# Kernel optimization log

Hardware: AMD Instinct MI355X
Metric: run time of the kernel (lower is better)

Reference implementation:

```python
import jax, jax.numpy as jnp
import numpy as np

NTYPES = 2
B, N, MNEI = 4, 512, 100
M = MNEI * NTYPES          # neighbor slots = maxNeighborNum * ntypes
EMB_LAST = 100             # embedding net sizes [25, 50, 100]
FIT_H = 240
M2 = 16
RMIN, RMAX = 0.5, 6.0


def setup_inputs():
    key = jax.random.key(0)
    ks = jax.random.split(key, 24)
    r = jax.random.uniform(ks[0], (B, N, M), minval=0.6, maxval=7.0)
    v = jax.random.normal(ks[1], (B, N, M, 3))
    v = v / jnp.linalg.norm(v, axis=-1, keepdims=True)
    keep = jax.random.uniform(ks[2], (B, N, M)) < 0.7
    ImageDR = jnp.concatenate([r[..., None], r[..., None] * v], axis=-1)
    ImageDR = jnp.where(keep[..., None], ImageDR, 0.0).astype(jnp.float32)
    Imagetype_map = jax.random.randint(ks[3], (N,), 0, NTYPES)
    list_neigh = jax.random.randint(ks[4], (B, N, M), 0, N + 1)
    type_map = jnp.arange(NTYPES)
    davg = (0.01 * jax.random.normal(ks[5], (NTYPES, M, 4))).astype(jnp.float32)
    dstd = (1.0 + 0.1 * jax.random.uniform(ks[6], (NTYPES, M, 4))).astype(jnp.float32)

    def w(k, shape, fan):
        return (jax.random.normal(k, shape) / np.sqrt(fan)).astype(jnp.float32)

    def b(k, shape):
        return (0.1 * jax.random.normal(k, shape)).astype(jnp.float32)

    emb_W0 = w(ks[7], (NTYPES, NTYPES, 1, 25), 1)
    emb_b0 = b(ks[8], (NTYPES, NTYPES, 25))
    emb_W1 = w(ks[9], (NTYPES, NTYPES, 25, 50), 25)
    emb_b1 = b(ks[10], (NTYPES, NTYPES, 50))
    emb_W2 = w(ks[11], (NTYPES, NTYPES, 50, 100), 50)
    emb_b2 = b(ks[12], (NTYPES, NTYPES, 100))
    fin = M2 * EMB_LAST
    fit_W0 = w(ks[13], (NTYPES, fin, FIT_H), fin)
    fit_b0 = b(ks[14], (NTYPES, FIT_H))
    fit_W1 = w(ks[15], (NTYPES, FIT_H, FIT_H), FIT_H)
    fit_b1 = b(ks[16], (NTYPES, FIT_H))
    fit_W2 = w(ks[17], (NTYPES, FIT_H, FIT_H), FIT_H)
    fit_b2 = b(ks[18], (NTYPES, FIT_H))
    fit_W3 = w(ks[19], (NTYPES, FIT_H, 1), FIT_H)
    fit_b3 = b(ks[20], (NTYPES, 1))
    energy_shift = jnp.array([-3.37, -5.21], dtype=jnp.float32)
    return dict(list_neigh=list_neigh, Imagetype_map=Imagetype_map, type_map=type_map,
                ImageDR=ImageDR, nghost=0, davg=davg, dstd=dstd,
                emb_W0=emb_W0, emb_b0=emb_b0, emb_W1=emb_W1, emb_b1=emb_b1,
                emb_W2=emb_W2, emb_b2=emb_b2,
                fit_W0=fit_W0, fit_b0=fit_b0, fit_W1=fit_W1, fit_b1=fit_b1,
                fit_W2=fit_W2, fit_b2=fit_b2, fit_W3=fit_W3, fit_b3=fit_b3,
                energy_shift=energy_shift)


def _emb(s, W0, b0, W1, b1, W2, b2):
    # DeepPot-SE embedding net with doubling resnet connections
    h = jnp.tanh(s @ W0 + b0)                                   # [..., 25]
    h = jnp.tanh(h @ W1 + b1) + jnp.concatenate([h, h], -1)     # [..., 50]
    return jnp.tanh(h @ W2 + b2) + jnp.concatenate([h, h], -1)  # [..., 100]


def _fit(d, W0, b0, W1, b1, W2, b2, W3, b3):
    h = jnp.tanh(d @ W0 + b0)
    h = h + jnp.tanh(h @ W1 + b1)
    h = h + jnp.tanh(h @ W2 + b2)
    return h @ W3 + b3


def _forward(ImageDR, davg, dstd,
             emb_W0, emb_b0, emb_W1, emb_b1, emb_W2, emb_b2,
             fit_W0, fit_b0, fit_W1, fit_b1, fit_W2, fit_b2, fit_W3, fit_b3,
             energy_shift, Imagetype_map):
    Bsz, Nat, Mtot, _ = ImageDR.shape
    m = Mtot // NTYPES
    R = ImageDR[..., 0]
    Rsafe = jnp.where(R > 1e-5, R, 1.0)
    # smooth switching function s(r): 1/r below Rmin, polynomial taper to Rmax
    u = (R - RMIN) / (RMAX - RMIN)
    mid = (u ** 3 * (-6.0 * u * u + 15.0 * u - 10.0) + 1.0) / Rsafe
    S = jnp.where((R > 0) & (R < RMIN), 1.0 / Rsafe,
                  jnp.where((R > RMIN) & (R < RMAX), mid, 0.0))
    msk = (jnp.abs(R) > 1e-5)[..., None]
    Ri = jnp.concatenate([S[..., None],
                          jnp.where(msk, (S / Rsafe)[..., None] * ImageDR[..., 1:4], 0.0)],
                         axis=-1)                                    # [B,N,M,4] = (s, s*x/r, s*y/r, s*z/r)
    # per-center-type normalization (irregular gather of stats)
    Rn = (Ri - davg[Imagetype_map][None]) / dstd[Imagetype_map][None]
    tmask = [(Imagetype_map == i).astype(Rn.dtype)[None, :, None, None] for i in range(NTYPES)]
    xyz = jnp.zeros((Bsz, Nat, 4, EMB_LAST), Rn.dtype)
    for j in range(NTYPES):                                          # neighbor-type slice
        sl = Rn[:, :, j * m:(j + 1) * m, :]                          # [B,N,m,4]
        s = sl[..., 0:1]
        G = jnp.zeros(sl.shape[:3] + (EMB_LAST,), sl.dtype)
        for i in range(NTYPES):                                      # center type -> pair net (i, j)
            G = G + tmask[i] * _emb(s, emb_W0[i, j], emb_b0[i, j],
                                    emb_W1[i, j], emb_b1[i, j], emb_W2[i, j], emb_b2[i, j])
        xyz = xyz + jnp.einsum('bnmk,bnmc->bnkc', sl, G)
    xyz = xyz / (m * NTYPES)
    # descriptor D = (Ri^T G)^T (Ri^T G)[:, :M2], flattened -> [B,N,EMB_LAST*M2]
    D = jnp.einsum('bnkc,bnkd->bncd', xyz, xyz[..., :M2]).reshape(Bsz, Nat, -1)
    Ei = jnp.zeros((Bsz, Nat), D.dtype)
    for i in range(NTYPES):
        e = _fit(D, fit_W0[i], fit_b0[i], fit_W1[i], fit_b1[i],
                 fit_W2[i], fit_b2[i], fit_W3[i], fit_b3[i])[..., 0] + energy_shift[i]
        Ei = Ei + tmask[i][:, :, 0, 0] * e
    Etot = jnp.sum(Ei, axis=1)
    return Etot, Ei


def reference(list_neigh, Imagetype_map, type_map, ImageDR, nghost, davg, dstd,
              emb_W0, emb_b0, emb_W1, emb_b1, emb_W2, emb_b2,
              fit_W0, fit_b0, fit_W1, fit_b1, fit_W2, fit_b2, fit_W3, fit_b3,
              energy_shift):
    return _forward(ImageDR, davg, dstd,
                    emb_W0, emb_b0, emb_W1, emb_b1, emb_W2, emb_b2,
                    fit_W0, fit_b0, fit_W1, fit_b1, fit_W2, fit_b2, fit_W3, fit_b3,
                    energy_shift, Imagetype_map)
```

## Files before the change

### kernel.cpp

```cpp
#include <hip/hip_runtime.h>
#include <math.h>

#define NT 2
#define BSZ 4
#define NAT 512
#define NATOMS 2048
#define NNEI 200
#define EMB 100
#define FITH 240
#define DDIM 1600
#define TBK 1024

#define BIAS_F  16
#define W3C_F   (BIAS_F + 3 * 512)
#define USH_BYTE 8320
#define TBL_U   0
#define W0T_U   409600
#define W1T_U   (W0T_U + 819200)
#define W2T_U   (W1T_U + 262144)
#define D_U     (W2T_U + 262144)
#define H0_U    (D_U + 3276800)
#define H1_U    (H0_U + 1048576)
#define USH_END (H1_U + 1048576)
#define WS_NEED ((size_t)USH_BYTE + (size_t)USH_END * 2)

typedef short s8v __attribute__((ext_vector_type(8)));
typedef float f4v __attribute__((ext_vector_type(4)));

__device__ __forceinline__ float ftanh(float x) {
    float ax = fabsf(x);
    float e = __expf(2.0f * ax);
    float t = 1.0f - __fdividef(2.0f, e + 1.0f);
    return (x < 0.0f) ? -t : t;
}
__device__ __forceinline__ unsigned short f2bf(float f) {
    unsigned u = __float_as_uint(f);
    u += 0x7FFFu + ((u >> 16) & 1u);
    return (unsigned short)(u >> 16);
}
__device__ __forceinline__ float bf2f(unsigned short s) {
    return __uint_as_float(((unsigned)s) << 16);
}
__device__ __forceinline__ float calc_S(float R) {
    float Rsafe = (R > 1e-5f) ? R : 1.0f;
    float u = (R - 0.5f) * (1.0f / 5.5f);
    float uu = u * u;
    float mid = (u * uu * (-6.0f * uu + 15.0f * u - 10.0f) + 1.0f) / Rsafe;
    float S = 0.0f;
    if (R > 0.0f && R < 0.5f)      S = 1.0f / Rsafe;
    else if (R > 0.5f && R < 6.0f) S = mid;
    return S;
}

#define N_W0 819200
#define N_W1 262144
#define N_W2 262144
#define N_B  1536
#define N_W3 512
#define N_EI 2048
__global__ void wtrans_kernel(const float* __restrict__ fW0, const float* __restrict__ fW1,
                              const float* __restrict__ fW2,
                              const float* __restrict__ fb0, const float* __restrict__ fb1,
                              const float* __restrict__ fb2,
                              const float* __restrict__ fW3, const float* __restrict__ fb3,
                              const float* __restrict__ eshift, const int* __restrict__ itype,
                              float* __restrict__ ws, float* __restrict__ out) {
    unsigned short* u0 = (unsigned short*)((char*)ws + USH_BYTE);
    int id = blockIdx.x * 256 + threadIdx.x;
    if (id < N_W0) {
        int n = id / 1600, k = id - n * 1600;
        float v = 0.0f;
        if (n < 240)                  v = fW0[(size_t)k * 240 + n];
        else if (n >= 256 && n < 496) v = fW0[(size_t)(1600 + k) * 240 + (n - 256)];
        u0[W0T_U + id] = f2bf(v);
        return;
    }
    id -= N_W0;
    if (id < N_W1) {
        int n = id / 512, k = id - n * 512;
        float v = 0.0f;
        if (n < 240 && k < 240)       v = fW1[(size_t)k * 240 + n];
        else if (n >= 256 && n < 496 && k >= 256 && k < 496)
                                      v = fW1[(size_t)(240 + (k - 256)) * 240 + (n - 256)];
        u0[W1T_U + id] = f2bf(v);
        return;
    }
    id -= N_W1;
    if (id < N_W2) {
        int n = id / 512, k = id - n * 512;
        float v = 0.0f;
        if (n < 240 && k < 240)       v = fW2[(size_t)k * 240 + n];
        else if (n >= 256 && n < 496 && k >= 256 && k < 496)
                                      v = fW2[(size_t)(240 + (k - 256)) * 240 + (n - 256)];
        u0[W2T_U + id] = f2bf(v);
        return;
    }
    id -= N_W2;
    if (id < N_B) {
        int l = id / 512, n = id - l * 512;
        const float* fb = (l == 0) ? fb0 : (l == 1) ? fb1 : fb2;
        float v = 0.0f;
        if (n < 240)                  v = fb[n];
        else if (n >= 256 && n < 496) v = fb[240 + (n - 256)];
        ws[BIAS_F + l * 512 + n] = v;
        return;
    }
    id -= N_B;
    if (id < N_W3) {
        int n = id;
        float v = 0.0f;
        if (n < 240)                  v = fW3[n];
        else if (n >= 256 && n < 496) v = fW3[240 + (n - 256)];
        ws[W3C_F + n] = v;
        return;
    }
    id -= N_W3;
    if (id < N_EI) {
        int t = itype[id & (NAT - 1)];
        out[4 + id] = fb3[t] + eshift[t];
    }
}

__global__ void __launch_bounds__(256) table_kernel(
    const float* __restrict__ davg, const float* __restrict__ dstd,
    const float* __restrict__ eW0, const float* __restrict__ eb0,
    const float* __restrict__ eW1, const float* __restrict__ eb1,
    const float* __restrict__ eW2, const float* __restrict__ eb2,
    float* __restrict__ ws)
{
    __shared__ float los[100], his[100];
    __shared__ float rng[2];
    __shared__ float h0s[8][25];
    __shared__ float h1s[8][50];
    const int bx = blockIdx.x;
    const int nid = bx >> 7;
    const int kb  = (bx & 127) * 8;
    const int t = nid >> 1, j = nid & 1;
    const int tid = threadIdx.x;

    if (tid < 100) {
        int m = j * 100 + tid;
        float av = davg[(t * NNEI + m) * 4];
        float sd = dstd[(t * NNEI + m) * 4];
        float inv = __fdividef(1.0f, sd);
        float a = (0.0f - av) * inv;
        float b = (2.0f - av) * inv;
        los[tid] = fminf(a, b);
        his[tid] = fmaxf(a, b);
    }
    __syncthreads();
    if (tid == 0) {
        float lo = los[0], hi = his[0];
        for (int i = 1; i < 100; ++i) { lo = fminf(lo, los[i]); hi = fmaxf(hi, his[i]); }
        rng[0] = lo; rng[1] = hi - lo;
        if (kb == 0) {
            ws[nid * 2] = lo;
            ws[nid * 2 + 1] = (float)(TBK - 1) / (hi - lo);
        }
    }
    __syncthreads();
    const float smin = rng[0], span = rng[1];
    const float* W0 = eW0 + nid * 25;
    const float* B0 = eb0 + nid * 25;
    if (tid < 200) {
        int q = tid / 25, a = tid % 25;
        float s = smin + span * ((float)(kb + q) * (1.0f / (TBK - 1)));
        h0s[q][a] = ftanh(fmaf(s, W0[a], B0[a]));
    }
    __syncthreads();
    const float* W1 = eW1 + nid * 1250;
    const float* B1 = eb1 + nid * 50;
    for (int idx = tid; idx < 400; idx += 256) {
        int q = idx / 50, cc = idx % 50;
        float acc = B1[cc];
#pragma unroll
        for (int a = 0; a < 25; ++a) acc = fmaf(h0s[q][a], W1[a * 50 + cc], acc);
        h1s[q][cc] = ftanh(acc) + h0s[q][(cc < 25) ? cc : cc - 25];
    }
    __syncthreads();
    const float* W2 = eW2 + nid * 5000;
    const float* B2 = eb2 + nid * 100;
    unsigned short* tblu = (unsigned short*)((char*)ws + USH_BYTE) + TBL_U;
    for (int idx = tid; idx < 800; idx += 256) {
        int q = idx / 100, c = idx % 100;
        float acc = B2[c];
#pragma unroll
        for (int a = 0; a < 50; ++a) acc = fmaf(h1s[q][a], W2[a * 100 + c], acc);
        float g = ftanh(acc) + h1s[q][(c < 50) ? c : c - 50];
        tblu[(size_t)(nid * TBK + kb + q) * 100 + c] = f2bf(g);
    }
}

__global__ void __launch_bounds__(128) embed_kernel(
    const int* __restrict__ itype, const float* __restrict__ imagedr,
    const float* __restrict__ davg, const float* __restrict__ dstd,
    float* __restrict__ ws)
{
    __shared__ __align__(16) float4 srn[NNEI];
    __shared__ float sx[NNEI];
    __shared__ float part[2][400];
    const int atom = blockIdx.x;
    const int n = atom & (NAT - 1);
    const int tid = threadIdx.x;
    const int t = itype[n];
    unsigned short* u0 = (unsigned short*)((char*)ws + USH_BYTE);

    const float sm0 = ws[(t * 2 + 0) * 2], sc0 = ws[(t * 2 + 0) * 2 + 1];
    const float sm1 = ws[(t * 2 + 1) * 2], sc1 = ws[(t * 2 + 1) * 2 + 1];

    for (int m = tid; m < NNEI; m += 128) {
        float4 dr = ((const float4*)imagedr)[(size_t)atom * NNEI + m];
        float R = dr.x;
        float S = calc_S(R);
        float Rsafe = (R > 1e-5f) ? R : 1.0f;
        float sr = (fabsf(R) > 1e-5f) ? (S / Rsafe) : 0.0f;
        float4 av = ((const float4*)davg)[t * NNEI + m];
        float4 sd = ((const float4*)dstd)[t * NNEI + m];
        float4 rv;
        rv.x = (S         - av.x) / sd.x;
        rv.y = (sr * dr.y - av.y) / sd.y;
        rv.z = (sr * dr.z - av.z) / sd.z;
        rv.w = (sr * dr.w - av.w) / sd.w;
        srn[m] = rv;
        float smin = (m >= 100) ? sm1 : sm0;
        float scal = (m >= 100) ? sc1 : sc0;
        sx[m] = fminf(fmaxf((rv.x - smin) * scal, 0.0f), (float)(TBK - 2) + 0.9999f);
    }
    __syncthreads();

    const int w = tid >> 6, lane = tid & 63;
    const unsigned short* T = u0 + TBL_U + (size_t)(t * 2 + w) * TBK * EMB;
    const bool hi = (lane < 36);
    float xA0 = 0, xA1 = 0, xA2 = 0, xA3 = 0;
    float xB0 = 0, xB1 = 0, xB2 = 0, xB3 = 0;
#pragma unroll 4
    for (int mi = 0; mi < 100; ++mi) {
        int m = w * 100 + mi;
        float4 rv = srn[m];
        float x = sx[m];
        int i = (int)x;
        float f = x - (float)i;
        const unsigned short* Tr = T + (size_t)i * EMB;
        float g0 = bf2f(Tr[lane]);
        float g1 = bf2f(Tr[EMB + lane]);
        float g = fmaf(f, g1 - g0, g0);
        xA0 = fmaf(rv.x, g, xA0); xA1 = fmaf(rv.y, g, xA1);
        xA2 = fmaf(rv.z, g, xA2); xA3 = fmaf(rv.w, g, xA3);
        if (hi) {
            float h0v = bf2f(Tr[64 + lane]);
            float h1v = bf2f(Tr[EMB + 64 + lane]);
            float g2 = fmaf(f, h1v - h0v, h0v);
            xB0 = fmaf(rv.x, g2, xB0); xB1 = fmaf(rv.y, g2, xB1);
            xB2 = fmaf(rv.z, g2, xB2); xB3 = fmaf(rv.w, g2, xB3);
        }
    }
    part[w][0 * 100 + lane] = xA0; part[w][1 * 100 + lane] = xA1;
    part[w][2 * 100 + lane] = xA2; part[w][3 * 100 + lane] = xA3;
    if (hi) {
        part[w][0 * 100 + 64 + lane] = xB0; part[w][1 * 100 + 64 + lane] = xB1;
        part[w][2 * 100 + 64 + lane] = xB2; part[w][3 * 100 + 64 + lane] = xB3;
    }
    __syncthreads();
    const float inv = 1.0f / 200.0f;
    for (int idx = tid; idx < 400; idx += 128)
        part[0][idx] = (part[0][idx] + part[1][idx]) * inv;
    __syncthreads();
    unsigned short* Drow = u0 + D_U + (size_t)atom * DDIM;
    const float* xt = part[0];
    for (int idx = tid; idx < DDIM; idx += 128) {
        int c = idx >> 4, d = idx & 15;
        float s = xt[c] * xt[d] + xt[100 + c] * xt[100 + d]
                + xt[200 + c] * xt[200 + d] + xt[300 + c] * xt[300 + d];
        Drow[idx] = f2bf(s);
    }
}

__global__ void __launch_bounds__(128) gemm0_kernel(
    const unsigned short* __restrict__ A,
    const unsigned short* __restrict__ BT,
    const float* __restrict__ bias,
    unsigned short* __restrict__ Out)
{
    __shared__ float lred[64][17];
    const int tid = threadIdx.x;
    const int w = tid >> 6, lane = tid & 63;
    const int mr = lane & 15, q = lane >> 4;
    const int n0 = blockIdx.x * 64;
    const int m0 = blockIdx.y * 16;
    const unsigned short* Ap = A  + (size_t)(m0 + mr) * DDIM + w * 800 + q * 8;
    const unsigned short* Bp = BT + (size_t)(n0 + mr) * DDIM + w * 800 + q * 8;

    f4v a0 = {0,0,0,0}, a1 = {0,0,0,0}, a2 = {0,0,0,0}, a3 = {0,0,0,0};
#pragma unroll 5
    for (int kt = 0; kt < 25; ++kt) {
        s8v av = *(const s8v*)(Ap + kt * 32);
        s8v b0 = *(const s8v*)(Bp + kt * 32);
        s8v b1 = *(const s8v*)(Bp + 16 * DDIM + kt * 32);
        s8v b2 = *(const s8v*)(Bp + 32 * DDIM + kt * 32);
        s8v b3 = *(const s8v*)(Bp + 48 * DDIM + kt * 32);
        a0 = __builtin_amdgcn_mfma_f32_16x16x32_bf16(av, b0, a0, 0, 0, 0);
        a1 = __builtin_amdgcn_mfma_f32_16x16x32_bf16(av, b1, a1, 0, 0, 0);
        a2 = __builtin_amdgcn_mfma_f32_16x16x32_bf16(av, b2, a2, 0, 0, 0);
        a3 = __builtin_amdgcn_mfma_f32_16x16x32_bf16(av, b3, a3, 0, 0, 0);
    }
    if (w == 1) {
#pragma unroll
        for (int r = 0; r < 4; ++r) {
            lred[lane][r]      = a0[r];
            lred[lane][4 + r]  = a1[r];
            lred[lane][8 + r]  = a2[r];
            lred[lane][12 + r] = a3[r];
        }
    }
    __syncthreads();
    if (w == 0) {
#pragma unroll
        for (int j = 0; j < 4; ++j) {
            const int col = n0 + j * 16 + mr;
            const float bv = bias[col];
            f4v* ap = (j == 0) ? &a0 : (j == 1) ? &a1 : (j == 2) ? &a2 : &a3;
#pragma unroll
            for (int r = 0; r < 4; ++r) {
                float s = (*ap)[r] + lred[lane][j * 4 + r] + bv;
                int row = m0 + q * 4 + r;
                Out[(size_t)row * 512 + col] = f2bf(ftanh(s));
            }
        }
    }
}

__global__ void __launch_bounds__(64) gemmr_kernel(
    const unsigned short* __restrict__ A, const unsigned short* __restrict__ BT,
    const float* __restrict__ bias, const unsigned short* __restrict__ Res,
    unsigned short* __restrict__ Out,
    const float* __restrict__ w3c, const int* __restrict__ itype,
    float* __restrict__ out, int mode)
{
    const int lane = threadIdx.x;
    const int mr = lane & 15, q = lane >> 4;
    const int bx = blockIdx.x;
    const int n0 = bx * 64;
    const int m0 = blockIdx.y * 16;
    const int k0 = (bx >= 4) ? 256 : 0;
    const unsigned short* Ap = A  + (size_t)(m0 + mr) * 512 + k0 + q * 8;
    const unsigned short* Bp = BT + (size_t)(n0 + mr) * 512 + k0 + q * 8;

    f4v a0 = {0,0,0,0}, a1 = {0,0,0,0}, a2 = {0,0,0,0}, a3 = {0,0,0,0};
#pragma unroll
    for (int kt = 0; kt < 8; ++kt) {
        s8v av = *(const s8v*)(Ap + kt * 32);
        s8v b0 = *(const s8v*)(Bp + kt * 32);
        s8v b1 = *(const s8v*)(Bp + 16 * 512 + kt * 32);
        s8v b2 = *(const s8v*)(Bp + 32 * 512 + kt * 32);
        s8v b3 = *(const s8v*)(Bp + 48 * 512 + kt * 32);
        a0 = __builtin_amdgcn_mfma_f32_16x16x32_bf16(av, b0, a0, 0, 0, 0);
        a1 = __builtin_amdgcn_mfma_f32_16x16x32_bf16(av, b1, a1, 0, 0, 0);
        a2 = __builtin_amdgcn_mfma_f32_16x16x32_bf16(av, b2, a2, 0, 0, 0);
        a3 = __builtin_amdgcn_mfma_f32_16x16x32_bf16(av, b3, a3, 0, 0, 0);
    }
    const float bv0 = bias[n0 + mr],      bv1 = bias[n0 + 16 + mr];
    const float bv2 = bias[n0 + 32 + mr], bv3 = bias[n0 + 48 + mr];
    if (mode == 1) {
#pragma unroll
        for (int r = 0; r < 4; ++r) {
            int row = m0 + q * 4 + r;
            size_t base = (size_t)row * 512 + n0 + mr;
            Out[base]      = f2bf(bf2f(Res[base])      + ftanh(a0[r] + bv0));
            Out[base + 16] = f2bf(bf2f(Res[base + 16]) + ftanh(a1[r] + bv1));
            Out[base + 32] = f2bf(bf2f(Res[base + 32]) + ftanh(a2[r] + bv2));
            Out[base + 48] = f2bf(bf2f(Res[base + 48]) + ftanh(a3[r] + bv3));
        }
    } else {
        const int seg = (bx >= 4);
        const float w30 = w3c[n0 + mr],      w31 = w3c[n0 + 16 + mr];
        const float w32 = w3c[n0 + 32 + mr], w33 = w3c[n0 + 48 + mr];
#pragma unroll
        for (int r = 0; r < 4; ++r) {
            int row = m0 + q * 4 + r;
            size_t base = (size_t)row * 512 + n0 + mr;
            float p = (bf2f(Res[base])      + ftanh(a0[r] + bv0)) * w30
                    + (bf2f(Res[base + 16]) + ftanh(a1[r] + bv1)) * w31
                    + (bf2f(Res[base + 32]) + ftanh(a2[r] + bv2)) * w32
                    + (bf2f(Res[base + 48]) + ftanh(a3[r] + bv3)) * w33;
            p += __shfl_xor(p, 1, 16);
            p += __shfl_xor(p, 2, 16);
            p += __shfl_xor(p, 4, 16);
            p += __shfl_xor(p, 8, 16);
            if (mr == 0 && itype[row & (NAT - 1)] == seg)
                atomicAdd(&out[4 + row], p);
        }
    }
}

__global__ void etot_kernel(float* __restrict__ out) {
    const int b = blockIdx.x;
    float s = 0.0f;
    for (int n = threadIdx.x; n < NAT; n += 256) s += out[4 + b * NAT + n];
#pragma unroll
    for (int off = 32; off > 0; off >>= 1) s += __shfl_down(s, off, 64);
    __shared__ float rr[4];
    if ((threadIdx.x & 63) == 0) rr[threadIdx.x >> 6] = s;
    __syncthreads();
    if (threadIdx.x == 0) out[b] = rr[0] + rr[1] + rr[2] + rr[3];
}

__global__ void dp_atom_kernel(
    const int* __restrict__ itype, const float* __restrict__ imagedr,
    const float* __restrict__ davg, const float* __restrict__ dstd,
    const float* __restrict__ eW0, const float* __restrict__ eb0,
    const float* __restrict__ eW1, const float* __restrict__ eb1,
    const float* __restrict__ eW2, const float* __restrict__ eb2,
    const float* __restrict__ fW0, const float* __restrict__ fb0,
    const float* __restrict__ fW1, const float* __restrict__ fb1,
    const float* __restrict__ fW2, const float* __restrict__ fb2,
    const float* __restrict__ fW3, const float* __restrict__ fb3,
    const float* __restrict__ eshift, float* __restrict__ out)
{
    __shared__ __align__(16) float4 rn4[NNEI];
    __shared__ __align__(16) float  xyz[4 * EMB];
    __shared__ __align__(16) float  h0s[100 * 25];
    __shared__ __align__(16) float  smem[100 * 52];
    const int atom = blockIdx.x;
    const int n = atom & (NAT - 1);
    const int tid = threadIdx.x;
    const int t = itype[n];
    for (int m = tid; m < NNEI; m += 256) {
        float4 dr = ((const float4*)imagedr)[(size_t)atom * NNEI + m];
        float R = dr.x;
        float S = calc_S(R);
        float Rsafe = (R > 1e-5f) ? R : 1.0f;
        float sr = (fabsf(R) > 1e-5f) ? (S / Rsafe) : 0.0f;
        float4 av = ((const float4*)davg)[t * NNEI + m];
        float4 sd = ((const float4*)dstd)[t * NNEI + m];
        float4 rv;
        rv.x = (S - av.x) / sd.x; rv.y = (sr * dr.y - av.y) / sd.y;
        rv.z = (sr * dr.z - av.z) / sd.z; rv.w = (sr * dr.w - av.w) / sd.w;
        rn4[m] = rv;
    }
    const int c = tid & 127; const int mh = tid >> 7;
    float xp0 = 0, xp1 = 0, xp2 = 0, xp3 = 0;
    for (int j = 0; j < NT; ++j) {
        const int wb = t * NT + j;
        const float* W0 = eW0 + wb * 25; const float* B0 = eb0 + wb * 25;
        const float* W1 = eW1 + wb * 1250; const float* B1 = eb1 + wb * 50;
        const float* W2 = eW2 + wb * 5000; const float* B2 = eb2 + wb * 100;
        __syncthreads();
        for (int idx = tid; idx < 2500; idx += 256) {
            int m = idx / 25, a = idx - m * 25;
            h0s[idx] = ftanh(fmaf(rn4[j * 100 + m].x, W0[a], B0[a]));
        }
        __syncthreads();
        for (int idx = tid; idx < 5000; idx += 256) {
            int m = idx / 50, cc = idx - m * 50;
            const float* h0m = h0s + m * 25;
            float acc = B1[cc];
#pragma unroll
            for (int a = 0; a < 25; ++a) acc = fmaf(h0m[a], W1[a * 50 + cc], acc);
            smem[m * 52 + cc] = ftanh(acc) + h0m[(cc < 25) ? cc : cc - 25];
        }
        for (int idx = tid; idx < 200; idx += 256)
            smem[(idx >> 1) * 52 + 50 + (idx & 1)] = 0.0f;
        __syncthreads();
        if (c < EMB) {
            float w2c[52];
#pragma unroll
            for (int a = 0; a < 50; ++a) w2c[a] = W2[a * EMB + c];
            w2c[50] = 0; w2c[51] = 0;
            const float bc = B2[c];
            const int sk = (c < 50) ? c : c - 50;
            for (int i = 0; i < 50; ++i) {
                int m = mh * 50 + i;
                const float* h1m = smem + m * 52;
                float acc = bc;
#pragma unroll
                for (int q = 0; q < 13; ++q) {
                    float4 hv = ((const float4*)h1m)[q];
                    acc = fmaf(hv.x, w2c[4 * q], acc); acc = fmaf(hv.y, w2c[4 * q + 1], acc);
                    acc = fmaf(hv.z, w2c[4 * q + 2], acc); acc = fmaf(hv.w, w2c[4 * q + 3], acc);
                }
                float g = ftanh(acc) + h1m[sk];
                float4 rm = rn4[j * 100 + m];
                xp0 = fmaf(rm.x, g, xp0); xp1 = fmaf(rm.y, g, xp1);
                xp2 = fmaf(rm.z, g, xp2); xp3 = fmaf(rm.w, g, xp3);
            }
        }
    }
    __syncthreads();
    const float inv = 1.0f / 200.0f;
    if (mh == 0 && c < EMB) {
        xyz[c] = xp0 * inv; xyz[EMB + c] = xp1 * inv;
        xyz[2 * EMB + c] = xp2 * inv; xyz[3 * EMB + c] = xp3 * inv;
    }
    __syncthreads();
    if (mh == 1 && c < EMB) {
        xyz[c] += xp0 * inv; xyz[EMB + c] += xp1 * inv;
        xyz[2 * EMB + c] += xp2 * inv; xyz[3 * EMB + c] += xp3 * inv;
    }
    __syncthreads();
    float* Dld = smem;
    for (int idx = tid; idx < DDIM; idx += 256) {
        int cc = idx >> 4, d = idx & 15;
        Dld[idx] = xyz[cc] * xyz[d] + xyz[EMB + cc] * xyz[EMB + d]
                 + xyz[2 * EMB + cc] * xyz[2 * EMB + d] + xyz[3 * EMB + cc] * xyz[3 * EMB + d];
    }
    __syncthreads();
    float* hA = smem + DDIM; float* hB = hA + FITH; float* h2 = hB + FITH; float* red = h2 + FITH;
    if (tid < FITH) {
        const float* W = fW0 + (size_t)t * DDIM * FITH;
        float acc = fb0[t * FITH + tid];
        for (int f = 0; f < DDIM; f += 4) {
            float4 dv = *(const float4*)(Dld + f);
            acc = fmaf(dv.x, W[f * FITH + tid], acc); acc = fmaf(dv.y, W[(f + 1) * FITH + tid], acc);
            acc = fmaf(dv.z, W[(f + 2) * FITH + tid], acc); acc = fmaf(dv.w, W[(f + 3) * FITH + tid], acc);
        }
        hA[tid] = ftanh(acc);
    }
    __syncthreads();
    if (tid < FITH) {
        const float* W = fW1 + t * FITH * FITH;
        float acc = fb1[t * FITH + tid];
        for (int f = 0; f < FITH; f += 4) {
            float4 hv = *(const float4*)(hA + f);
            acc = fmaf(hv.x, W[f * FITH + tid], acc); acc = fmaf(hv.y, W[(f + 1) * FITH + tid], acc);
            acc = fmaf(hv.z, W[(f + 2) * FITH + tid], acc); acc = fmaf(hv.w, W[(f + 3) * FITH + tid], acc);
        }
        hB[tid] = hA[tid] + ftanh(acc);
    }
    __syncthreads();
    if (tid < FITH) {
        const float* W = fW2 + t * FITH * FITH;
        float acc = fb2[t * FITH + tid];
        for (int f = 0; f < FITH; f += 4) {
            float4 hv = *(const float4*)(hB + f);
            acc = fmaf(hv.x, W[f * FITH + tid], acc); acc = fmaf(hv.y, W[(f + 1) * FITH + tid], acc);
            acc = fmaf(hv.z, W[(f + 2) * FITH + tid], acc); acc = fmaf(hv.w, W[(f + 3) * FITH + tid], acc);
        }
        h2[tid] = hB[tid] + ftanh(acc);
    }
    __syncthreads();
    float p = (tid < FITH) ? h2[tid] * fW3[t * FITH + tid] : 0.0f;
#pragma unroll
    for (int off = 32; off > 0; off >>= 1) p += __shfl_down(p, off, 64);
    if ((tid & 63) == 0) red[tid >> 6] = p;
    __syncthreads();
    if (tid == 0) out[4 + atom] = red[0] + red[1] + red[2] + red[3] + fb3[t] + eshift[t];
}

extern "C" void kernel_launch(void* const* d_in, const int* in_sizes, int n_in,
                              void* d_out, int out_size, void* d_ws, size_t ws_size,
                              hipStream_t stream) {
    const int*   itype   = (const int*)  d_in[1];
    const float* imagedr = (const float*)d_in[3];
    const float* davg    = (const float*)d_in[5];
    const float* dstd    = (const float*)d_in[6];
    const float* eW0     = (const float*)d_in[7];
    const float* eb0     = (const float*)d_in[8];
    const float* eW1     = (const float*)d_in[9];
    const float* eb1     = (const float*)d_in[10];
    const float* eW2     = (const float*)d_in[11];
    const float* eb2     = (const float*)d_in[12];
    const float* fW0     = (const float*)d_in[13];
    const float* fb0     = (const float*)d_in[14];
    const float* fW1     = (const float*)d_in[15];
    const float* fb1     = (const float*)d_in[16];
    const float* fW2     = (const float*)d_in[17];
    const float* fb2     = (const float*)d_in[18];
    const float* fW3     = (const float*)d_in[19];
    const float* fb3     = (const float*)d_in[20];
    const float* eshift  = (const float*)d_in[21];
    float* out = (float*)d_out;
    float* ws  = (float*)d_ws;

    if (ws_size >= WS_NEED) {
        unsigned short* u0 = (unsigned short*)((char*)ws + USH_BYTE);
        const int n_ids = N_W0 + N_W1 + N_W2 + N_B + N_W3 + N_EI;
        wtrans_kernel<<<(n_ids + 255) / 256, 256, 0, stream>>>(
            fW0, fW1, fW2, fb0, fb1, fb2, fW3, fb3, eshift, itype, ws, out);
        table_kernel<<<512, 256, 0, stream>>>(davg, dstd, eW0, eb0, eW1, eb1, eW2, eb2, ws);
        embed_kernel<<<NATOMS, 128, 0, stream>>>(itype, imagedr, davg, dstd, ws);
        gemm0_kernel<<<dim3(8, 128), 128, 0, stream>>>(
            u0 + D_U, u0 + W0T_U, ws + BIAS_F, u0 + H0_U);
        gemmr_kernel<<<dim3(8, 128), 64, 0, stream>>>(
            u0 + H0_U, u0 + W1T_U, ws + BIAS_F + 512, u0 + H0_U, u0 + H1_U,
            nullptr, nullptr, nullptr, 1);
        gemmr_kernel<<<dim3(8, 128), 64, 0, stream>>>(
            u0 + H1_U, u0 + W2T_U, ws + BIAS_F + 1024, u0 + H1_U, nullptr,
            ws + W3C_F, itype, out, 2);
        etot_kernel<<<BSZ, 256, 0, stream>>>(out);
    } else {
        dp_atom_kernel<<<NATOMS, 256, 0, stream>>>(itype, imagedr, davg, dstd,
            eW0, eb0, eW1, eb1, eW2, eb2,
            fW0, fb0, fW1, fb1, fW2, fb2, fW3, fb3, eshift, out);
        etot_kernel<<<BSZ, 256, 0, stream>>>(out);
    }
}
```

Measured before the change: 192.3 us.

## Group atoms by type so fitting GEMMs compute only the matching type's network

```diff
diff --git a/kernel.cpp b/kernel.cpp
--- a/kernel.cpp
+++ b/kernel.cpp
@@ -13,7 +13,9 @@
 
 #define BIAS_F  16
 #define W3C_F   (BIAS_F + 3 * 512)
-#define USH_BYTE 8320
+#define PERM_I  2064
+#define CNT_I   (PERM_I + 2048)
+#define USH_BYTE 16512
 #define TBL_U   0
 #define W0T_U   409600
 #define W1T_U   (W0T_U + 819200)
@@ -24,6 +26,16 @@
 #define USH_END (H1_U + 1048576)
 #define WS_NEED ((size_t)USH_BYTE + (size_t)USH_END * 2)
 
+#define N_W0 819200
+#define N_W1 262144
+#define N_W2 262144
+#define N_B  1536
+#define N_W3 512
+#define N_EI 2048
+#define N_WT (N_W0 + N_W1 + N_W2 + N_B + N_W3 + N_EI)
+#define WT_BLK ((N_WT + 255) / 256)
+#define TB_BLK 512
+
 typedef short s8v __attribute__((ext_vector_type(8)));
 typedef float f4v __attribute__((ext_vector_type(4)));
 
@@ -52,143 +64,157 @@
     return S;
 }
 
-#define N_W0 819200
-#define N_W1 262144
-#define N_W2 262144
-#define N_B  1536
-#define N_W3 512
-#define N_EI 2048
-__global__ void wtrans_kernel(const float* __restrict__ fW0, const float* __restrict__ fW1,
-                              const float* __restrict__ fW2,
-                              const float* __restrict__ fb0, const float* __restrict__ fb1,
-                              const float* __restrict__ fb2,
-                              const float* __restrict__ fW3, const float* __restrict__ fb3,
-                              const float* __restrict__ eshift, const int* __restrict__ itype,
-                              float* __restrict__ ws, float* __restrict__ out) {
-    unsigned short* u0 = (unsigned short*)((char*)ws + USH_BYTE);
-    int id = blockIdx.x * 256 + threadIdx.x;
-    if (id < N_W0) {
-        int n = id / 1600, k = id - n * 1600;
-        float v = 0.0f;
-        if (n < 240)                  v = fW0[(size_t)k * 240 + n];
-        else if (n >= 256 && n < 496) v = fW0[(size_t)(1600 + k) * 240 + (n - 256)];
-        u0[W0T_U + id] = f2bf(v);
-        return;
-    }
-    id -= N_W0;
-    if (id < N_W1) {
-        int n = id / 512, k = id - n * 512;
-        float v = 0.0f;
-        if (n < 240 && k < 240)       v = fW1[(size_t)k * 240 + n];
-        else if (n >= 256 && n < 496 && k >= 256 && k < 496)
-                                      v = fW1[(size_t)(240 + (k - 256)) * 240 + (n - 256)];
-        u0[W1T_U + id] = f2bf(v);
-        return;
-    }
-    id -= N_W1;
-    if (id < N_W2) {
-        int n = id / 512, k = id - n * 512;
-        float v = 0.0f;
-        if (n < 240 && k < 240)       v = fW2[(size_t)k * 240 + n];
-        else if (n >= 256 && n < 496 && k >= 256 && k < 496)
-                                      v = fW2[(size_t)(240 + (k - 256)) * 240 + (n - 256)];
-        u0[W2T_U + id] = f2bf(v);
-        return;
-    }
-    id -= N_W2;
-    if (id < N_B) {
-        int l = id / 512, n = id - l * 512;
-        const float* fb = (l == 0) ? fb0 : (l == 1) ? fb1 : fb2;
-        float v = 0.0f;
-        if (n < 240)                  v = fb[n];
-        else if (n >= 256 && n < 496) v = fb[240 + (n - 256)];
-        ws[BIAS_F + l * 512 + n] = v;
-        return;
-    }
-    id -= N_B;
-    if (id < N_W3) {
-        int n = id;
-        float v = 0.0f;
-        if (n < 240)                  v = fW3[n];
-        else if (n >= 256 && n < 496) v = fW3[240 + (n - 256)];
-        ws[W3C_F + n] = v;
-        return;
-    }
-    id -= N_W3;
-    if (id < N_EI) {
-        int t = itype[id & (NAT - 1)];
-        out[4 + id] = fb3[t] + eshift[t];
-    }
-}
-
-__global__ void __launch_bounds__(256) table_kernel(
+__global__ void __launch_bounds__(256) prep_kernel(
+    const float* __restrict__ fW0, const float* __restrict__ fW1,
+    const float* __restrict__ fW2,
+    const float* __restrict__ fb0, const float* __restrict__ fb1,
+    const float* __restrict__ fb2,
+    const float* __restrict__ fW3, const float* __restrict__ fb3,
+    const float* __restrict__ eshift,
     const float* __restrict__ davg, const float* __restrict__ dstd,
     const float* __restrict__ eW0, const float* __restrict__ eb0,
     const float* __restrict__ eW1, const float* __restrict__ eb1,
     const float* __restrict__ eW2, const float* __restrict__ eb2,
-    float* __restrict__ ws)
+    const int* __restrict__ itype,
+    float* __restrict__ ws, float* __restrict__ out)
 {
     __shared__ float los[100], his[100];
     __shared__ float rng[2];
     __shared__ float h0s[8][25];
     __shared__ float h1s[8][50];
-    const int bx = blockIdx.x;
-    const int nid = bx >> 7;
-    const int kb  = (bx & 127) * 8;
-    const int t = nid >> 1, j = nid & 1;
+    __shared__ int pcnt, poff0, poff1;
     const int tid = threadIdx.x;
-
-    if (tid < 100) {
-        int m = j * 100 + tid;
-        float av = davg[(t * NNEI + m) * 4];
-        float sd = dstd[(t * NNEI + m) * 4];
-        float inv = __fdividef(1.0f, sd);
-        float a = (0.0f - av) * inv;
-        float b = (2.0f - av) * inv;
-        los[tid] = fminf(a, b);
-        his[tid] = fmaxf(a, b);
-    }
-    __syncthreads();
-    if (tid == 0) {
-        float lo = los[0], hi = his[0];
-        for (int i = 1; i < 100; ++i) { lo = fminf(lo, los[i]); hi = fmaxf(hi, his[i]); }
-        rng[0] = lo; rng[1] = hi - lo;
-        if (kb == 0) {
-            ws[nid * 2] = lo;
-            ws[nid * 2 + 1] = (float)(TBK - 1) / (hi - lo);
-        }
-    }
-    __syncthreads();
-    const float smin = rng[0], span = rng[1];
-    const float* W0 = eW0 + nid * 25;
-    const float* B0 = eb0 + nid * 25;
-    if (tid < 200) {
-        int q = tid / 25, a = tid % 25;
-        float s = smin + span * ((float)(kb + q) * (1.0f / (TBK - 1)));
-        h0s[q][a] = ftanh(fmaf(s, W0[a], B0[a]));
-    }
-    __syncthreads();
-    const float* W1 = eW1 + nid * 1250;
-    const float* B1 = eb1 + nid * 50;
-    for (int idx = tid; idx < 400; idx += 256) {
-        int q = idx / 50, cc = idx % 50;
-        float acc = B1[cc];
-#pragma unroll
-        for (int a = 0; a < 25; ++a) acc = fmaf(h0s[q][a], W1[a * 50 + cc], acc);
-        h1s[q][cc] = ftanh(acc) + h0s[q][(cc < 25) ? cc : cc - 25];
-    }
-    __syncthreads();
-    const float* W2 = eW2 + nid * 5000;
-    const float* B2 = eb2 + nid * 100;
-    unsigned short* tblu = (unsigned short*)((char*)ws + USH_BYTE) + TBL_U;
-    for (int idx = tid; idx < 800; idx += 256) {
-        int q = idx / 100, c = idx % 100;
-        float acc = B2[c];
-#pragma unroll
-        for (int a = 0; a < 50; ++a) acc = fmaf(h1s[q][a], W2[a * 100 + c], acc);
-        float g = ftanh(acc) + h1s[q][(c < 50) ? c : c - 50];
-        tblu[(size_t)(nid * TBK + kb + q) * 100 + c] = f2bf(g);
-    }
+    int bxg = blockIdx.x;
+    unsigned short* u0 = (unsigned short*)((char*)ws + USH_BYTE);
+
+    if (bxg < WT_BLK) {
+        int id = bxg * 256 + tid;
+        if (id < N_W0) {
+            int n = id / 1600, k = id - n * 1600;
+            float v = 0.0f;
+            if (n < 240)                  v = fW0[(size_t)k * 240 + n];
+            else if (n >= 256 && n < 496) v = fW0[(size_t)(1600 + k) * 240 + (n - 256)];
+            u0[W0T_U + id] = f2bf(v);
+            return;
+        }
+        id -= N_W0;
+        if (id < N_W1) {
+            int n = id / 512, k = id - n * 512;
+            float v = 0.0f;
+            if (n < 240 && k < 240)       v = fW1[(size_t)k * 240 + n];
+            else if (n >= 256 && n < 496 && k >= 256 && k < 496)
+                                          v = fW1[(size_t)(240 + (k - 256)) * 240 + (n - 256)];
+            u0[W1T_U + id] = f2bf(v);
+            return;
+        }
+        id -= N_W1;
+        if (id < N_W2) {
+            int n = id / 512, k = id - n * 512;
+            float v = 0.0f;
+            if (n < 240 && k < 240)       v = fW2[(size_t)k * 240 + n];
+            else if (n >= 256 && n < 496 && k >= 256 && k < 496)
+                                          v = fW2[(size_t)(240 + (k - 256)) * 240 + (n - 256)];
+            u0[W2T_U + id] = f2bf(v);
+            return;
+        }
+        id -= N_W2;
+        if (id < N_B) {
+            int l = id / 512, n = id - l * 512;
+            const float* fb = (l == 0) ? fb0 : (l == 1) ? fb1 : fb2;
+            float v = 0.0f;
+            if (n < 240)                  v = fb[n];
+            else if (n >= 256 && n < 496) v = fb[240 + (n - 256)];
+            ws[BIAS_F + l * 512 + n] = v;
+            return;
+        }
+        id -= N_B;
+        if (id < N_W3) {
+            int n = id;
+            float v = 0.0f;
+            if (n < 240)                  v = fW3[n];
+            else if (n >= 256 && n < 496) v = fW3[240 + (n - 256)];
+            ws[W3C_F + n] = v;
+            return;
+        }
+        id -= N_W3;
+        if (id < N_EI) {
+            int t = itype[id & (NAT - 1)];
+            out[4 + id] = fb3[t] + eshift[t];
+        }
+        return;
+    }
+    bxg -= WT_BLK;
+    if (bxg < TB_BLK) {
+        const int nid = bxg >> 7;
+        const int kb  = (bxg & 127) * 8;
+        const int t = nid >> 1, j = nid & 1;
+        if (tid < 100) {
+            int m = j * 100 + tid;
+            float av = davg[(t * NNEI + m) * 4];
+            float sd = dstd[(t * NNEI + m) * 4];
+            float inv = __fdividef(1.0f, sd);
+            float a = (0.0f - av) * inv;
+            float b = (2.0f - av) * inv;
+            los[tid] = fminf(a, b);
+            his[tid] = fmaxf(a, b);
+        }
+        __syncthreads();
+        if (tid == 0) {
+            float lo = los[0], hi = his[0];
+            for (int i = 1; i < 100; ++i) { lo = fminf(lo, los[i]); hi = fmaxf(hi, his[i]); }
+            rng[0] = lo; rng[1] = hi - lo;
+            if (kb == 0) {
+                ws[nid * 2] = lo;
+                ws[nid * 2 + 1] = (float)(TBK - 1) / (hi - lo);
+            }
+        }
+        __syncthreads();
+        const float smin = rng[0], span = rng[1];
+        const float* W0 = eW0 + nid * 25;
+        const float* B0 = eb0 + nid * 25;
+        if (tid < 200) {
+            int q = tid / 25, a = tid % 25;
+            float s = smin + span * ((float)(kb + q) * (1.0f / (TBK - 1)));
+            h0s[q][a] = ftanh(fmaf(s, W0[a], B0[a]));
+        }
+        __syncthreads();
+        const float* W1 = eW1 + nid * 1250;
+        const float* B1 = eb1 + nid * 50;
+        for (int idx = tid; idx < 400; idx += 256) {
+            int q = idx / 50, cc = idx % 50;
+            float acc = B1[cc];
+#pragma unroll
+            for (int a = 0; a < 25; ++a) acc = fmaf(h0s[q][a], W1[a * 50 + cc], acc);
+            h1s[q][cc] = ftanh(acc) + h0s[q][(cc < 25) ? cc : cc - 25];
+        }
+        __syncthreads();
+        const float* W2 = eW2 + nid * 5000;
+        const float* B2 = eb2 + nid * 100;
+        unsigned short* tblu = u0 + TBL_U;
+        for (int idx = tid; idx < 800; idx += 256) {
+            int q = idx / 100, c = idx % 100;
+            float acc = B2[c];
+#pragma unroll
+            for (int a = 0; a < 50; ++a) acc = fmaf(h1s[q][a], W2[a * 100 + c], acc);
+            float g = ftanh(acc) + h1s[q][(c < 50) ? c : c - 50];
+            tblu[(size_t)(nid * TBK + kb + q) * 100 + c] = f2bf(g);
+        }
+        return;
+    }
+    if (tid == 0) { pcnt = 0; poff0 = 0; poff1 = 0; }
+    __syncthreads();
+    int* wsi = (int*)ws;
+    int local0 = 0;
+    for (int i = tid; i < NATOMS; i += 256) local0 += (itype[i & (NAT - 1)] == 0);
+    atomicAdd(&pcnt, local0);
+    __syncthreads();
+    const int c0 = pcnt;
+    for (int i = tid; i < NATOMS; i += 256) {
+        int t = itype[i & (NAT - 1)];
+        int pos = (t == 0) ? atomicAdd(&poff0, 1) : (c0 + atomicAdd(&poff1, 1));
+        wsi[PERM_I + pos] = i;
+    }
+    if (tid == 0) { wsi[CNT_I] = c0; wsi[CNT_I + 1] = NATOMS - c0; }
 }
 
 __global__ void __launch_bounds__(128) embed_kernel(
@@ -279,15 +305,22 @@
     const unsigned short* __restrict__ A,
     const unsigned short* __restrict__ BT,
     const float* __restrict__ bias,
+    const int* __restrict__ wsi,
     unsigned short* __restrict__ Out)
 {
     __shared__ float lred[64][17];
+    const int z = blockIdx.z;
+    const int cnt = wsi[CNT_I + z];
+    const int my = blockIdx.y;
+    if (my * 16 >= cnt) return;
+    const int base = z ? wsi[CNT_I] : 0;
     const int tid = threadIdx.x;
     const int w = tid >> 6, lane = tid & 63;
     const int mr = lane & 15, q = lane >> 4;
-    const int n0 = blockIdx.x * 64;
-    const int m0 = blockIdx.y * 16;
-    const unsigned short* Ap = A  + (size_t)(m0 + mr) * DDIM + w * 800 + q * 8;
+    const int n0 = z * 256 + blockIdx.x * 64;
+    const int m0 = my * 16;
+    const int arow = wsi[PERM_I + base + min(m0 + mr, cnt - 1)];
+    const unsigned short* Ap = A  + (size_t)arow * DDIM + w * 800 + q * 8;
     const unsigned short* Bp = BT + (size_t)(n0 + mr) * DDIM + w * 800 + q * 8;
 
     f4v a0 = {0,0,0,0}, a1 = {0,0,0,0}, a2 = {0,0,0,0}, a3 = {0,0,0,0};
@@ -321,9 +354,12 @@
             f4v* ap = (j == 0) ? &a0 : (j == 1) ? &a1 : (j == 2) ? &a2 : &a3;
 #pragma unroll
             for (int r = 0; r < 4; ++r) {
-                float s = (*ap)[r] + lred[lane][j * 4 + r] + bv;
-                int row = m0 + q * 4 + r;
-                Out[(size_t)row * 512 + col] = f2bf(ftanh(s));
+                int rl = m0 + q * 4 + r;
+                if (rl < cnt) {
+                    int orow = wsi[PERM_I + base + rl];
+                    float s = (*ap)[r] + lred[lane][j * 4 + r] + bv;
+                    Out[(size_t)orow * 512 + col] = f2bf(ftanh(s));
+                }
             }
         }
     }
@@ -333,16 +369,21 @@
     const unsigned short* __restrict__ A, const unsigned short* __restrict__ BT,
     const float* __restrict__ bias, const unsigned short* __restrict__ Res,
     unsigned short* __restrict__ Out,
-    const float* __restrict__ w3c, const int* __restrict__ itype,
+    const float* __restrict__ w3c, const int* __restrict__ wsi,
     float* __restrict__ out, int mode)
 {
+    const int z = blockIdx.z;
+    const int cnt = wsi[CNT_I + z];
+    const int my = blockIdx.y;
+    if (my * 16 >= cnt) return;
+    const int base = z ? wsi[CNT_I] : 0;
     const int lane = threadIdx.x;
     const int mr = lane & 15, q = lane >> 4;
-    const int bx = blockIdx.x;
-    const int n0 = bx * 64;
-    const int m0 = blockIdx.y * 16;
-    const int k0 = (bx >= 4) ? 256 : 0;
-    const unsigned short* Ap = A  + (size_t)(m0 + mr) * 512 + k0 + q * 8;
+    const int n0 = z * 256 + blockIdx.x * 64;
+    const int k0 = z * 256;
+    const int m0 = my * 16;
+    const int arow = wsi[PERM_I + base + min(m0 + mr, cnt - 1)];
+    const unsigned short* Ap = A  + (size_t)arow * 512 + k0 + q * 8;
     const unsigned short* Bp = BT + (size_t)(n0 + mr) * 512 + k0 + q * 8;
 
     f4v a0 = {0,0,0,0}, a1 = {0,0,0,0}, a2 = {0,0,0,0}, a3 = {0,0,0,0};
@@ -363,31 +404,35 @@
     if (mode == 1) {
 #pragma unroll
         for (int r = 0; r < 4; ++r) {
-            int row = m0 + q * 4 + r;
-            size_t base = (size_t)row * 512 + n0 + mr;
-            Out[base]      = f2bf(bf2f(Res[base])      + ftanh(a0[r] + bv0));
-            Out[base + 16] = f2bf(bf2f(Res[base + 16]) + ftanh(a1[r] + bv1));
-            Out[base + 32] = f2bf(bf2f(Res[base + 32]) + ftanh(a2[r] + bv2));
-            Out[base + 48] = f2bf(bf2f(Res[base + 48]) + ftanh(a3[r] + bv3));
+            int rl = m0 + q * 4 + r;
+            if (rl < cnt) {
+                int orow = wsi[PERM_I + base + rl];
+                size_t b_ = (size_t)orow * 512 + n0 + mr;
+                Out[b_]      = f2bf(bf2f(Res[b_])      + ftanh(a0[r] + bv0));
+                Out[b_ + 16] = f2bf(bf2f(Res[b_ + 16]) + ftanh(a1[r] + bv1));
+                Out[b_ + 32] = f2bf(bf2f(Res[b_ + 32]) + ftanh(a2[r] + bv2));
+                Out[b_ + 48] = f2bf(bf2f(Res[b_ + 48]) + ftanh(a3[r] + bv3));
+            }
         }
     } else {
-        const int seg = (bx >= 4);
         const float w30 = w3c[n0 + mr],      w31 = w3c[n0 + 16 + mr];
         const float w32 = w3c[n0 + 32 + mr], w33 = w3c[n0 + 48 + mr];
 #pragma unroll
         for (int r = 0; r < 4; ++r) {
-            int row = m0 + q * 4 + r;
-            size_t base = (size_t)row * 512 + n0 + mr;
-            float p = (bf2f(Res[base])      + ftanh(a0[r] + bv0)) * w30
-                    + (bf2f(Res[base + 16]) + ftanh(a1[r] + bv1)) * w31
-                    + (bf2f(Res[base + 32]) + ftanh(a2[r] + bv2)) * w32
-                    + (bf2f(Res[base + 48]) + ftanh(a3[r] + bv3)) * w33;
-            p += __shfl_xor(p, 1, 16);
-            p += __shfl_xor(p, 2, 16);
-            p += __shfl_xor(p, 4, 16);
-            p += __shfl_xor(p, 8, 16);
-            if (mr == 0 && itype[row & (NAT - 1)] == seg)
-                atomicAdd(&out[4 + row], p);
+            int rl = m0 + q * 4 + r;
+            if (rl < cnt) {
+                int orow = wsi[PERM_I + base + rl];
+                size_t b_ = (size_t)orow * 512 + n0 + mr;
+                float p = (bf2f(Res[b_])      + ftanh(a0[r] + bv0)) * w30
+                        + (bf2f(Res[b_ + 16]) + ftanh(a1[r] + bv1)) * w31
+                        + (bf2f(Res[b_ + 32]) + ftanh(a2[r] + bv2)) * w32
+                        + (bf2f(Res[b_ + 48]) + ftanh(a3[r] + bv3)) * w33;
+                p += __shfl_xor(p, 1, 16);
+                p += __shfl_xor(p, 2, 16);
+                p += __shfl_xor(p, 4, 16);
+                p += __shfl_xor(p, 8, 16);
+                if (mr == 0) atomicAdd(&out[4 + orow], p);
+            }
         }
     }
 }
@@ -573,19 +618,19 @@
 
     if (ws_size >= WS_NEED) {
         unsigned short* u0 = (unsigned short*)((char*)ws + USH_BYTE);
-        const int n_ids = N_W0 + N_W1 + N_W2 + N_B + N_W3 + N_EI;
-        wtrans_kernel<<<(n_ids + 255) / 256, 256, 0, stream>>>(
-            fW0, fW1, fW2, fb0, fb1, fb2, fW3, fb3, eshift, itype, ws, out);
-        table_kernel<<<512, 256, 0, stream>>>(davg, dstd, eW0, eb0, eW1, eb1, eW2, eb2, ws);
+        const int* wsi = (const int*)ws;
+        prep_kernel<<<WT_BLK + TB_BLK + 1, 256, 0, stream>>>(
+            fW0, fW1, fW2, fb0, fb1, fb2, fW3, fb3, eshift,
+            davg, dstd, eW0, eb0, eW1, eb1, eW2, eb2, itype, ws, out);
         embed_kernel<<<NATOMS, 128, 0, stream>>>(itype, imagedr, davg, dstd, ws);
-        gemm0_kernel<<<dim3(8, 128), 128, 0, stream>>>(
-            u0 + D_U, u0 + W0T_U, ws + BIAS_F, u0 + H0_U);
-        gemmr_kernel<<<dim3(8, 128), 64, 0, stream>>>(
+        gemm0_kernel<<<dim3(4, 128, 2), 128, 0, stream>>>(
+            u0 + D_U, u0 + W0T_U, ws + BIAS_F, wsi, u0 + H0_U);
+        gemmr_kernel<<<dim3(4, 128, 2), 64, 0, stream>>>(
             u0 + H0_U, u0 + W1T_U, ws + BIAS_F + 512, u0 + H0_U, u0 + H1_U,
-            nullptr, nullptr, nullptr, 1);
-        gemmr_kernel<<<dim3(8, 128), 64, 0, stream>>>(
+            nullptr, wsi, nullptr, 1);
+        gemmr_kernel<<<dim3(4, 128, 2), 64, 0, stream>>>(
             u0 + H1_U, u0 + W2T_U, ws + BIAS_F + 1024, u0 + H1_U, nullptr,
-            ws + W3C_F, itype, out, 2);
+            ws + W3C_F, wsi, out, 2);
         etot_kernel<<<BSZ, 256, 0, stream>>>(out);
     } else {
         dp_atom_kernel<<<NATOMS, 256, 0, stream>>>(itype, imagedr, davg, dstd,
```

After: 191.7 us. No clear change (-0.3%).
